# Performance work log

Hardware: AMD Instinct MI355X
Metric: run time of the kernel (lower is better)

The kernel has to match this reference:

```python
import jax, jax.numpy as jnp
import numpy as np

N, D, E, T = 30000, 256, 300000, 2
HID, OUT, HEADS = 64, 256, 8


def setup_inputs() -> dict:
    key = jax.random.key(0)
    ks = jax.random.split(key, 16)
    g = lambda k, shape, fan_in: jax.random.normal(k, shape, jnp.float32) / np.sqrt(fan_in)
    inp = {
        'x': jax.random.normal(ks[0], (N, D), jnp.float32),
        'edge_index': jax.random.randint(ks[1], (T, 2, E), 0, N, jnp.int32),
        'w1_l': g(ks[2], (T, D, HEADS * HID), D),
        'b1_l': jnp.zeros((T, HEADS * HID), jnp.float32),
        'w1_r': g(ks[3], (T, D, HEADS * HID), D),
        'b1_r': jnp.zeros((T, HEADS * HID), jnp.float32),
        'att1': g(ks[4], (T, HEADS, HID), HID),
        'bias1': jnp.zeros((T, HEADS * HID), jnp.float32),
        'w2_l': g(ks[5], (T, HEADS * HID, OUT), HEADS * HID),
        'b2_l': jnp.zeros((T, OUT), jnp.float32),
        'w2_r': g(ks[6], (T, HEADS * HID, OUT), HEADS * HID),
        'b2_r': jnp.zeros((T, OUT), jnp.float32),
        'att2': g(ks[7], (T, 1, OUT), OUT),
        'bias2': jnp.zeros((T, OUT), jnp.float32),
        'w_lin': g(ks[8], (OUT, OUT), OUT),
        'b_lin': jnp.zeros((OUT,), jnp.float32),
    }
    return inp


def _gatv2(x, src, dst, w_l, b_l, w_r, b_r, att, bias, num_nodes):
    # GATv2Conv: e = att . leaky_relu(W_l x_src + W_r x_dst); softmax over in-edges of dst;
    # out = scatter_add(alpha * W_l x_src) per destination; concat heads + bias.
    H, C = att.shape
    xl = (x @ w_l + b_l).reshape(num_nodes, H, C)
    xr = (x @ w_r + b_r).reshape(num_nodes, H, C)
    h = jax.nn.leaky_relu(xl[src] + xr[dst], 0.2)      # [E, H, C]
    e = jnp.einsum('ehc,hc->eh', h, att)               # [E, H]
    m = jax.ops.segment_max(e, dst, num_segments=num_nodes)
    p = jnp.exp(e - m[dst])
    s = jax.ops.segment_sum(p, dst, num_segments=num_nodes)
    alpha = p / s[dst]                                 # softmax over neighbors
    out = jax.ops.segment_sum(xl[src] * alpha[:, :, None], dst, num_segments=num_nodes)
    return out.reshape(num_nodes, H * C) + bias


def reference(x, edge_index, w1_l, b1_l, w1_r, b1_r, att1, bias1,
              w2_l, b2_l, w2_r, b2_r, att2, bias2, w_lin, b_lin):
    n = x.shape[0]
    loop = jnp.arange(n, dtype=edge_index.dtype)  # GATv2Conv default add_self_loops=True
    srcs, dsts = [], []
    for t in range(edge_index.shape[0]):
        srcs.append(jnp.concatenate([edge_index[t, 0], loop]))
        dsts.append(jnp.concatenate([edge_index[t, 1], loop]))

    # conv1 (heads=8, concat) with HeteroConv aggr='sum'
    h1 = jnp.zeros((n, w1_l.shape[2]), x.dtype)
    for t in range(len(srcs)):
        h1 = h1 + _gatv2(x, srcs[t], dsts[t], w1_l[t], b1_l[t], w1_r[t], b1_r[t], att1[t], bias1[t], n)
    h1 = jax.nn.elu(h1)

    # conv2 (heads=1, concat=False -> mean over 1 head == identity)
    h2 = jnp.zeros((n, w2_l.shape[2]), x.dtype)
    for t in range(len(srcs)):
        h2 = h2 + _gatv2(h1, srcs[t], dsts[t], w2_l[t], b2_l[t], w2_r[t], b2_r[t], att2[t], bias2[t], n)
    h2 = jax.nn.elu(h2)

    return h2 @ w_lin + b_lin
```

## Files before the change

### kernel.cpp

```cpp
#include <hip/hip_runtime.h>
#include <math.h>

#define N_NODES 30000
#define D_IN    256
#define E_EDGES 300000
#define T_TYPES 2
#define HEADS   8
#define HID     64
#define F1      512
#define OUT_F   256
#define EP      (E_EDGES + N_NODES)

typedef __attribute__((ext_vector_type(8))) short bf16x8;
typedef __attribute__((ext_vector_type(4))) float f32x4;

__device__ __forceinline__ unsigned short f2bf(float f) {
    unsigned u = __float_as_uint(f);
    unsigned r = 0x7fffu + ((u >> 16) & 1u);
    return (unsigned short)((u + r) >> 16);
}
__device__ __forceinline__ float bf2f(unsigned short h) {
    return __uint_as_float(((unsigned)h) << 16);
}

#define PREP_W1   (8 * 65536)
#define PREP_W2   (4 * 131072)
#define PREP_WL   65536
#define PREP_CNT  (T_TYPES * N_NODES)
#define PREP_TOT  (PREP_W1 + PREP_W2 + PREP_WL + PREP_CNT)

__global__ void prep_kernel(const float* __restrict__ w1_l, const float* __restrict__ w1_r,
                            const float* __restrict__ w2_l, const float* __restrict__ w2_r,
                            const float* __restrict__ w_lin,
                            unsigned short* __restrict__ wt1h, unsigned short* __restrict__ wt1l,
                            unsigned short* __restrict__ wt2h, unsigned short* __restrict__ wt2l,
                            unsigned short* __restrict__ wtLh, unsigned short* __restrict__ wtLl,
                            int* __restrict__ count) {
    int idx = blockIdx.x * blockDim.x + threadIdx.x;
    if (idx < PREP_W1) {
        int n = idx & 255, k = (idx >> 8) & 255, mat = idx >> 16;
        int h = mat & 1, lr = (mat >> 1) & 1, t = mat >> 2;
        const float* src = lr ? w1_r : w1_l;
        float v = src[(size_t)t * 256 * 512 + (size_t)k * 512 + h * 256 + n];
        unsigned short hi = f2bf(v);
        unsigned short lo = f2bf(v - bf2f(hi));
        size_t o = (size_t)mat * 65536 + (size_t)n * 256 + k;
        wt1h[o] = hi; wt1l[o] = lo;
        return;
    }
    idx -= PREP_W1;
    if (idx < PREP_W2) {
        int n = idx & 255, k = (idx >> 8) & 511, mat = idx >> 17;
        int lr = mat & 1, t = mat >> 1;
        const float* src = lr ? w2_r : w2_l;
        float v = src[(size_t)t * 512 * 256 + (size_t)k * 256 + n];
        unsigned short hi = f2bf(v);
        unsigned short lo = f2bf(v - bf2f(hi));
        size_t o = (size_t)mat * 131072 + (size_t)n * 512 + k;
        wt2h[o] = hi; wt2l[o] = lo;
        return;
    }
    idx -= PREP_W2;
    if (idx < PREP_WL) {
        int n = idx & 255, k = idx >> 8;
        float v = w_lin[k * 256 + n];
        unsigned short hi = f2bf(v);
        unsigned short lo = f2bf(v - bf2f(hi));
        size_t o = (size_t)n * 256 + k;
        wtLh[o] = hi; wtLl[o] = lo;
        return;
    }
    idx -= PREP_WL;
    if (idx < PREP_CNT) count[idx] = 0;
}

__global__ void hist_kernel(const int* __restrict__ ei, int* __restrict__ count) {
    int idx = blockIdx.x * blockDim.x + threadIdx.x;
    if (idx >= T_TYPES * EP) return;
    int t = idx / EP, i = idx - t * EP;
    int dst = (i < E_EDGES) ? ei[t * 2 * E_EDGES + E_EDGES + i] : (i - E_EDGES);
    atomicAdd(&count[t * N_NODES + dst], 1);
}

#define SCAN_NB 30

__global__ __launch_bounds__(256) void scan_bsum_kernel(const int* __restrict__ cnt,
                                                        int* __restrict__ bsum) {
    int t = blockIdx.y, b = blockIdx.x;
    const int* c = cnt + t * N_NODES;
    int i0 = b * 1024 + threadIdx.x * 4;
    int s = 0;
    #pragma unroll
    for (int j = 0; j < 4; ++j) { int i = i0 + j; if (i < N_NODES) s += c[i]; }
    #pragma unroll
    for (int m = 1; m < 64; m <<= 1) s += __shfl_xor(s, m);
    __shared__ int wsum[4];
    int l = threadIdx.x & 63, w = threadIdx.x >> 6;
    if (l == 0) wsum[w] = s;
    __syncthreads();
    if (threadIdx.x == 0) bsum[t * SCAN_NB + b] = wsum[0] + wsum[1] + wsum[2] + wsum[3];
}

__global__ void scan_base_kernel(int* __restrict__ bsum) {
    int t = threadIdx.x;
    if (t >= T_TYPES) return;
    int acc = 0;
    for (int b = 0; b < SCAN_NB; ++b) {
        int v = bsum[t * SCAN_NB + b];
        bsum[t * SCAN_NB + b] = acc;
        acc += v;
    }
}

__global__ __launch_bounds__(256) void scan_write_kernel(int* __restrict__ cnt,
                                                         const int* __restrict__ bsum,
                                                         int* __restrict__ off) {
    int t = blockIdx.y, b = blockIdx.x;
    int tid = threadIdx.x;
    int* c = cnt + t * N_NODES;
    int* o = off + t * (N_NODES + 1);
    int i0 = b * 1024 + tid * 4;
    int v[4]; int s = 0;
    #pragma unroll
    for (int j = 0; j < 4; ++j) { int i = i0 + j; v[j] = (i < N_NODES) ? c[i] : 0; s += v[j]; }
    __shared__ int ps[256];
    ps[tid] = s;
    __syncthreads();
    for (int ofs = 1; ofs < 256; ofs <<= 1) {
        int x = (tid >= ofs) ? ps[tid - ofs] : 0;
        __syncthreads();
        ps[tid] += x;
        __syncthreads();
    }
    int base = bsum[t * SCAN_NB + b] + ps[tid] - s;
    #pragma unroll
    for (int j = 0; j < 4; ++j) {
        int i = i0 + j;
        if (i < N_NODES) { o[i] = base; base += v[j]; c[i] = 0; }
    }
    if (b == 0 && tid == 0) o[N_NODES] = EP;
}

__global__ void scatter_kernel(const int* __restrict__ ei, const int* __restrict__ offsets,
                               int* __restrict__ cursor, int* __restrict__ csr_src) {
    int idx = blockIdx.x * blockDim.x + threadIdx.x;
    if (idx >= T_TYPES * EP) return;
    int t = idx / EP, i = idx - t * EP;
    int src, dst;
    if (i < E_EDGES) {
        src = ei[t * 2 * E_EDGES + i];
        dst = ei[t * 2 * E_EDGES + E_EDGES + i];
    } else {
        src = dst = i - E_EDGES;
    }
    int pos = offsets[t * (N_NODES + 1) + dst] + atomicAdd(&cursor[t * N_NODES + dst], 1);
    csr_src[t * EP + pos] = src;
}

__global__ __launch_bounds__(256) void gemm_mfma_kernel(
        const float* __restrict__ A, int lda,
        const unsigned short* __restrict__ Bh0, const unsigned short* __restrict__ Bl0,
        const float* __restrict__ bias0, float* __restrict__ C0,
        const unsigned short* __restrict__ Bh1, const unsigned short* __restrict__ Bl1,
        const float* __restrict__ bias1, float* __restrict__ C1,
        int M, int K) {
    const unsigned short* Bh = blockIdx.y ? Bh1 : Bh0;
    const unsigned short* Bl = blockIdx.y ? Bl1 : Bl0;
    const float* bias = blockIdx.y ? bias1 : bias0;
    float* C = blockIdx.y ? C1 : C0;

    __shared__ unsigned short Ah_s[64 * 32], Al_s[64 * 32];
    __shared__ unsigned short Bh_s[256 * 32], Bl_s[256 * 32];
    int t = threadIdx.x;
    int row0 = blockIdx.x * 64;
    int w = t >> 6;
    int l = t & 63;
    int fm = l & 15;
    int fg = l >> 4;

    f32x4 acc[4][4];
    const f32x4 zf = {0.f, 0.f, 0.f, 0.f};
    #pragma unroll
    for (int i = 0; i < 4; ++i)
        #pragma unroll
        for (int j = 0; j < 4; ++j) acc[i][j] = zf;

    int ar = t >> 3;
    int af = t & 7;
    int bn = t >> 2;
    int bb = t & 3;

    for (int k0 = 0; k0 < K; k0 += 32) {
        #pragma unroll
        for (int v = 0; v < 2; ++v) {
            int r = v * 32 + ar;
            int rg = row0 + r;
            float4 a4 = make_float4(0.f, 0.f, 0.f, 0.f);
            if (rg < M) a4 = *(const float4*)&A[(size_t)rg * lda + k0 + af * 4];
            ushort4 hi, lo;
            hi.x = f2bf(a4.x); lo.x = f2bf(a4.x - bf2f(hi.x));
            hi.y = f2bf(a4.y); lo.y = f2bf(a4.y - bf2f(hi.y));
            hi.z = f2bf(a4.z); lo.z = f2bf(a4.z - bf2f(hi.z));
            hi.w = f2bf(a4.w); lo.w = f2bf(a4.w - bf2f(hi.w));
            int ke = (af * 4) ^ (((r >> 1) & 3) << 3);
            *(ushort4*)&Ah_s[r * 32 + ke] = hi;
            *(ushort4*)&Al_s[r * 32 + ke] = lo;
        }
        #pragma unroll
        for (int g = 0; g < 4; ++g) {
            int n = g * 64 + bn;
            *(uint4*)&Bh_s[n * 32 + bb * 8] = *(const uint4*)&Bh[(size_t)n * K + k0 + bb * 8];
            *(uint4*)&Bl_s[n * 32 + bb * 8] = *(const uint4*)&Bl[(size_t)n * K + k0 + bb * 8];
        }
        __syncthreads();
        bf16x8 ah[4], al[4], bh[4], bl[4];
        #pragma unroll
        for (int i = 0; i < 4; ++i) {
            int r = i * 16 + fm;
            int ke = (fg * 8) ^ (((r >> 1) & 3) << 3);
            ah[i] = *(const bf16x8*)&Ah_s[r * 32 + ke];
            al[i] = *(const bf16x8*)&Al_s[r * 32 + ke];
        }
        #pragma unroll
        for (int j = 0; j < 4; ++j) {
            int n = w * 64 + j * 16 + fm;
            bh[j] = *(const bf16x8*)&Bh_s[n * 32 + fg * 8];
            bl[j] = *(const bf16x8*)&Bl_s[n * 32 + fg * 8];
        }
        #pragma unroll
        for (int i = 0; i < 4; ++i)
            #pragma unroll
            for (int j = 0; j < 4; ++j) {
                acc[i][j] = __builtin_amdgcn_mfma_f32_16x16x32_bf16(ah[i], bh[j], acc[i][j], 0, 0, 0);
                acc[i][j] = __builtin_amdgcn_mfma_f32_16x16x32_bf16(ah[i], bl[j], acc[i][j], 0, 0, 0);
                acc[i][j] = __builtin_amdgcn_mfma_f32_16x16x32_bf16(al[i], bh[j], acc[i][j], 0, 0, 0);
            }
        __syncthreads();
    }
    #pragma unroll
    for (int j = 0; j < 4; ++j) {
        int col = w * 64 + j * 16 + fm;
        float bv = bias[col];
        #pragma unroll
        for (int i = 0; i < 4; ++i) {
            #pragma unroll
            for (int q = 0; q < 4; ++q) {
                int rg = row0 + i * 16 + fg * 4 + q;
                if (rg < M) C[(size_t)rg * 256 + col] = acc[i][j][q] + bv;
            }
        }
    }
}

template <int RW, int MODE>
__global__ __launch_bounds__(256) void gat_edge_kernel(
        const float* __restrict__ xl, const float* __restrict__ xr,
        const float* __restrict__ att,
        const int* __restrict__ offs, const int* __restrict__ csr,
        float* __restrict__ out, int ldo,
        const float* __restrict__ eb0, const float* __restrict__ eb1) {
    int wave = (blockIdx.x * blockDim.x + threadIdx.x) >> 6;
    int lane = threadIdx.x & 63;
    if (wave >= N_NODES) return;
    int d = wave;
    int q4 = lane * 4;
    float attr[4], xrr[4];
    *(float4*)&attr[0] = *(const float4*)&att[q4];
    *(float4*)&xrr[0]  = *(const float4*)&xr[(size_t)d * 256 + q4];
    float m = -INFINITY, s = 0.f;
    float acc[4] = {0.f, 0.f, 0.f, 0.f};
    int p0 = offs[d], p1 = offs[d + 1];
    int p = p0;
    for (; p + 2 <= p1; p += 2) {
        int s0 = csr[p], s1 = csr[p + 1];
        float xv0[4], xv1[4];
        *(float4*)&xv0[0] = *(const float4*)&xl[(size_t)s0 * 256 + q4];
        *(float4*)&xv1[0] = *(const float4*)&xl[(size_t)s1 * 256 + q4];
        float e0 = 0.f, e1 = 0.f;
        #pragma unroll
        for (int q = 0; q < 4; ++q) {
            float h0 = xv0[q] + xrr[q];
            float h1 = xv1[q] + xrr[q];
            h0 = (h0 > 0.f) ? h0 : 0.2f * h0;
            h1 = (h1 > 0.f) ? h1 : 0.2f * h1;
            e0 += attr[q] * h0;
            e1 += attr[q] * h1;
        }
        #pragma unroll
        for (int msk = 1; msk < RW; msk <<= 1) {
            e0 += __shfl_xor(e0, msk);
            e1 += __shfl_xor(e1, msk);
        }
        float mn = fmaxf(m, e0);
        float sc = __expf(m - mn);
        float pe = __expf(e0 - mn);
        s = s * sc + pe;
        #pragma unroll
        for (int q = 0; q < 4; ++q) acc[q] = acc[q] * sc + pe * xv0[q];
        m = mn;
        mn = fmaxf(m, e1);
        sc = __expf(m - mn);
        pe = __expf(e1 - mn);
        s = s * sc + pe;
        #pragma unroll
        for (int q = 0; q < 4; ++q) acc[q] = acc[q] * sc + pe * xv1[q];
        m = mn;
    }
    if (p < p1) {
        int s0 = csr[p];
        float xv0[4];
        *(float4*)&xv0[0] = *(const float4*)&xl[(size_t)s0 * 256 + q4];
        float e0 = 0.f;
        #pragma unroll
        for (int q = 0; q < 4; ++q) {
            float h0 = xv0[q] + xrr[q];
            h0 = (h0 > 0.f) ? h0 : 0.2f * h0;
            e0 += attr[q] * h0;
        }
        #pragma unroll
        for (int msk = 1; msk < RW; msk <<= 1) e0 += __shfl_xor(e0, msk);
        float mn = fmaxf(m, e0);
        float sc = __expf(m - mn);
        float pe = __expf(e0 - mn);
        s = s * sc + pe;
        #pragma unroll
        for (int q = 0; q < 4; ++q) acc[q] = acc[q] * sc + pe * xv0[q];
        m = mn;
    }
    float inv = 1.f / s;
    float* dp = &out[(size_t)d * ldo + q4];
    if (MODE == 0) {
        *(float4*)dp = make_float4(acc[0] * inv, acc[1] * inv, acc[2] * inv, acc[3] * inv);
    } else {
        #pragma unroll
        for (int q = 0; q < 4; ++q) {
            float v = dp[q] + acc[q] * inv + eb0[q4 + q] + eb1[q4 + q];
            dp[q] = (v > 0.f) ? v : (__expf(v) - 1.f);
        }
    }
}

extern "C" void kernel_launch(void* const* d_in, const int* in_sizes, int n_in,
                              void* d_out, int out_size, void* d_ws, size_t ws_size,
                              hipStream_t stream) {
    const float* x      = (const float*)d_in[0];
    const int*   ei     = (const int*)d_in[1];
    const float* w1_l   = (const float*)d_in[2];
    const float* b1_l   = (const float*)d_in[3];
    const float* w1_r   = (const float*)d_in[4];
    const float* b1_r   = (const float*)d_in[5];
    const float* att1   = (const float*)d_in[6];
    const float* bias1  = (const float*)d_in[7];
    const float* w2_l   = (const float*)d_in[8];
    const float* b2_l   = (const float*)d_in[9];
    const float* w2_r   = (const float*)d_in[10];
    const float* b2_r   = (const float*)d_in[11];
    const float* att2   = (const float*)d_in[12];
    const float* bias2  = (const float*)d_in[13];
    const float* w_lin  = (const float*)d_in[14];
    const float* b_lin  = (const float*)d_in[15];
    float* out = (float*)d_out;

    float* h1   = (float*)d_ws;
    float* bufA = h1 + (size_t)N_NODES * F1;
    float* bufB = bufA + (size_t)N_NODES * OUT_F;
    unsigned short* wt1h = (unsigned short*)(bufB + (size_t)N_NODES * OUT_F);
    unsigned short* wt1l = wt1h + 8 * 65536;
    unsigned short* wt2h = wt1l + 8 * 65536;
    unsigned short* wt2l = wt2h + 4 * 131072;
    unsigned short* wtLh = wt2l + 4 * 131072;
    unsigned short* wtLl = wtLh + 65536;
    int* count   = (int*)(wtLl + 65536);
    int* offsets = count + T_TYPES * N_NODES;
    int* bsum    = offsets + T_TYPES * (N_NODES + 1);
    int* csr     = bsum + T_TYPES * SCAN_NB;
    float* h2 = out;

    prep_kernel<<<(PREP_TOT + 255) / 256, 256, 0, stream>>>(
        w1_l, w1_r, w2_l, w2_r, w_lin, wt1h, wt1l, wt2h, wt2l, wtLh, wtLl, count);

    int eblocks = (T_TYPES * EP + 255) / 256;
    hist_kernel<<<eblocks, 256, 0, stream>>>(ei, count);
    dim3 sgrid(SCAN_NB, T_TYPES);
    scan_bsum_kernel<<<sgrid, 256, 0, stream>>>(count, bsum);
    scan_base_kernel<<<1, 64, 0, stream>>>(bsum);
    scan_write_kernel<<<sgrid, 256, 0, stream>>>(count, bsum, offsets);
    scatter_kernel<<<eblocks, 256, 0, stream>>>(ei, offsets, count, csr);

    int gat_blocks = N_NODES / 4;
    dim3 ggrid((N_NODES + 63) / 64, 2);
    dim3 ggrid1((N_NODES + 63) / 64, 1);

    for (int t = 0; t < T_TYPES; ++t) {
        for (int hh = 0; hh < 2; ++hh) {
            int co = hh * 256;
            int ml = (t * 2 + 0) * 2 + hh, mr = (t * 2 + 1) * 2 + hh;
            gemm_mfma_kernel<<<ggrid, 256, 0, stream>>>(
                x, D_IN,
                wt1h + (size_t)ml * 65536, wt1l + (size_t)ml * 65536, b1_l + t * F1 + co, bufA,
                wt1h + (size_t)mr * 65536, wt1l + (size_t)mr * 65536, b1_r + t * F1 + co, bufB,
                N_NODES, D_IN);
            if (t == 0)
                gat_edge_kernel<16, 0><<<gat_blocks, 256, 0, stream>>>(
                    bufA, bufB, att1 + t * F1 + co, offsets + t * (N_NODES + 1),
                    csr + (size_t)t * EP, h1 + co, F1, nullptr, nullptr);
            else
                gat_edge_kernel<16, 2><<<gat_blocks, 256, 0, stream>>>(
                    bufA, bufB, att1 + t * F1 + co, offsets + t * (N_NODES + 1),
                    csr + (size_t)t * EP, h1 + co, F1, bias1 + co, bias1 + F1 + co);
        }
    }

    for (int t = 0; t < T_TYPES; ++t) {
        int ml = t * 2 + 0, mr = t * 2 + 1;
        gemm_mfma_kernel<<<ggrid, 256, 0, stream>>>(
            h1, F1,
            wt2h + (size_t)ml * 131072, wt2l + (size_t)ml * 131072, b2_l + t * OUT_F, bufA,
            wt2h + (size_t)mr * 131072, wt2l + (size_t)mr * 131072, b2_r + t * OUT_F, bufB,
            N_NODES, F1);
        if (t == 0)
            gat_edge_kernel<64, 0><<<gat_blocks, 256, 0, stream>>>(
                bufA, bufB, att2 + t * OUT_F, offsets + t * (N_NODES + 1),
                csr + (size_t)t * EP, h2, OUT_F, nullptr, nullptr);
        else
            gat_edge_kernel<64, 2><<<gat_blocks, 256, 0, stream>>>(
                bufA, bufB, att2 + t * OUT_F, offsets + t * (N_NODES + 1),
                csr + (size_t)t * EP, h2, OUT_F, bias2, bias2 + OUT_F);
    }

    hipMemcpyAsync(bufA, h2, (size_t)N_NODES * OUT_F * sizeof(float),
                   hipMemcpyDeviceToDevice, stream);
    gemm_mfma_kernel<<<ggrid1, 256, 0, stream>>>(
        bufA, OUT_F, wtLh, wtLl, b_lin, out, wtLh, wtLl, b_lin, out, N_NODES, OUT_F);
}
```

Measured before the change: 905.5 us.

## Register-prefetch GEMM tiles, swizzle B in LDS, and emit split-bf16 h2 from the edge kernel

The GEMM kernel now loads the next K-tile of A and B into registers while computing the current one, overlapping global loads with MFMA work. It also XOR-swizzles the B tile in shared memory to avoid bank conflicts and adds a launch-bounds occupancy hint. The last GAT edge kernel writes h2 directly as pre-split bf16 hi/lo arrays, so the final linear GEMM reads them without conversion and the device-to-device copy is removed. In exchange, register pressure rises from the prefetch buffers, and h1 storage is reused to hold the split h2.

Result: slower. 1.480 ms (+63.4%).

```diff
diff --git a/kernel.cpp b/kernel.cpp
--- a/kernel.cpp
+++ b/kernel.cpp
@@ -157,8 +157,9 @@
     csr_src[t * EP + pos] = src;
 }
 
-__global__ __launch_bounds__(256) void gemm_mfma_kernel(
-        const float* __restrict__ A, int lda,
+template <int ASPLIT>
+__global__ __launch_bounds__(256, 3) void gemm_mfma_kernel(
+        const void* __restrict__ A0v, const void* __restrict__ A1v, int lda,
         const unsigned short* __restrict__ Bh0, const unsigned short* __restrict__ Bl0,
         const float* __restrict__ bias0, float* __restrict__ C0,
         const unsigned short* __restrict__ Bh1, const unsigned short* __restrict__ Bl1,
@@ -168,6 +169,9 @@
     const unsigned short* Bl = blockIdx.y ? Bl1 : Bl0;
     const float* bias = blockIdx.y ? bias1 : bias0;
     float* C = blockIdx.y ? C1 : C0;
+    const float* Af          = (const float*)A0v;
+    const unsigned short* Ah = (const unsigned short*)A0v;
+    const unsigned short* Al = (const unsigned short*)A1v;
 
     __shared__ unsigned short Ah_s[64 * 32], Al_s[64 * 32];
     __shared__ unsigned short Bh_s[256 * 32], Bl_s[256 * 32];
@@ -185,55 +189,90 @@
         #pragma unroll
         for (int j = 0; j < 4; ++j) acc[i][j] = zf;
 
-    int ar = t >> 3;
-    int af = t & 7;
-    int bn = t >> 2;
-    int bb = t & 3;
-
-    for (int k0 = 0; k0 < K; k0 += 32) {
-        #pragma unroll
-        for (int v = 0; v < 2; ++v) {
-            int r = v * 32 + ar;
-            int rg = row0 + r;
-            float4 a4 = make_float4(0.f, 0.f, 0.f, 0.f);
-            if (rg < M) a4 = *(const float4*)&A[(size_t)rg * lda + k0 + af * 4];
-            ushort4 hi, lo;
-            hi.x = f2bf(a4.x); lo.x = f2bf(a4.x - bf2f(hi.x));
-            hi.y = f2bf(a4.y); lo.y = f2bf(a4.y - bf2f(hi.y));
-            hi.z = f2bf(a4.z); lo.z = f2bf(a4.z - bf2f(hi.z));
-            hi.w = f2bf(a4.w); lo.w = f2bf(a4.w - bf2f(hi.w));
-            int ke = (af * 4) ^ (((r >> 1) & 3) << 3);
-            *(ushort4*)&Ah_s[r * 32 + ke] = hi;
-            *(ushort4*)&Al_s[r * 32 + ke] = lo;
+    int ar = t >> 3, af = t & 7;
+    int ar1 = t >> 2, ac1 = t & 3;
+    int bn = t >> 2, bb = t & 3;
+
+    float4 aP[2];
+    uint4 ahP, alP;
+    uint4 bhP[4], blP[4];
+
+    auto load_tile = [&](int k0) {
+        if constexpr (ASPLIT == 0) {
+            #pragma unroll
+            for (int v = 0; v < 2; ++v) {
+                int rg = row0 + v * 32 + ar;
+                aP[v] = make_float4(0.f, 0.f, 0.f, 0.f);
+                if (rg < M) aP[v] = *(const float4*)&Af[(size_t)rg * lda + k0 + af * 4];
+            }
+        } else {
+            int rg = row0 + ar1;
+            ahP = make_uint4(0, 0, 0, 0);
+            alP = make_uint4(0, 0, 0, 0);
+            if (rg < M) {
+                ahP = *(const uint4*)&Ah[(size_t)rg * lda + k0 + ac1 * 8];
+                alP = *(const uint4*)&Al[(size_t)rg * lda + k0 + ac1 * 8];
+            }
         }
         #pragma unroll
         for (int g = 0; g < 4; ++g) {
             int n = g * 64 + bn;
-            *(uint4*)&Bh_s[n * 32 + bb * 8] = *(const uint4*)&Bh[(size_t)n * K + k0 + bb * 8];
-            *(uint4*)&Bl_s[n * 32 + bb * 8] = *(const uint4*)&Bl[(size_t)n * K + k0 + bb * 8];
-        }
+            bhP[g] = *(const uint4*)&Bh[(size_t)n * K + k0 + bb * 8];
+            blP[g] = *(const uint4*)&Bl[(size_t)n * K + k0 + bb * 8];
+        }
+    };
+
+    load_tile(0);
+    for (int k0 = 0; k0 < K; k0 += 32) {
+        if constexpr (ASPLIT == 0) {
+            #pragma unroll
+            for (int v = 0; v < 2; ++v) {
+                int r = v * 32 + ar;
+                ushort4 hi, lo;
+                hi.x = f2bf(aP[v].x); lo.x = f2bf(aP[v].x - bf2f(hi.x));
+                hi.y = f2bf(aP[v].y); lo.y = f2bf(aP[v].y - bf2f(hi.y));
+                hi.z = f2bf(aP[v].z); lo.z = f2bf(aP[v].z - bf2f(hi.z));
+                hi.w = f2bf(aP[v].w); lo.w = f2bf(aP[v].w - bf2f(hi.w));
+                int ke = (af * 4) ^ (((r >> 1) & 3) << 3);
+                *(ushort4*)&Ah_s[r * 32 + ke] = hi;
+                *(ushort4*)&Al_s[r * 32 + ke] = lo;
+            }
+        } else {
+            int ke = (ac1 * 8) ^ (((ar1 >> 1) & 3) << 3);
+            *(uint4*)&Ah_s[ar1 * 32 + ke] = ahP;
+            *(uint4*)&Al_s[ar1 * 32 + ke] = alP;
+        }
+        #pragma unroll
+        for (int g = 0; g < 4; ++g) {
+            int n = g * 64 + bn;
+            int ke = (bb * 8) ^ (((n >> 1) & 3) << 3);
+            *(uint4*)&Bh_s[n * 32 + ke] = bhP[g];
+            *(uint4*)&Bl_s[n * 32 + ke] = blP[g];
+        }
+        if (k0 + 32 < K) load_tile(k0 + 32);
         __syncthreads();
-        bf16x8 ah[4], al[4], bh[4], bl[4];
+        bf16x8 ahf[4], alf[4], bhf[4], blf[4];
         #pragma unroll
         for (int i = 0; i < 4; ++i) {
             int r = i * 16 + fm;
             int ke = (fg * 8) ^ (((r >> 1) & 3) << 3);
-            ah[i] = *(const bf16x8*)&Ah_s[r * 32 + ke];
-            al[i] = *(const bf16x8*)&Al_s[r * 32 + ke];
+            ahf[i] = *(const bf16x8*)&Ah_s[r * 32 + ke];
+            alf[i] = *(const bf16x8*)&Al_s[r * 32 + ke];
         }
         #pragma unroll
         for (int j = 0; j < 4; ++j) {
             int n = w * 64 + j * 16 + fm;
-            bh[j] = *(const bf16x8*)&Bh_s[n * 32 + fg * 8];
-            bl[j] = *(const bf16x8*)&Bl_s[n * 32 + fg * 8];
+            int ke = (fg * 8) ^ (((n >> 1) & 3) << 3);
+            bhf[j] = *(const bf16x8*)&Bh_s[n * 32 + ke];
+            blf[j] = *(const bf16x8*)&Bl_s[n * 32 + ke];
         }
         #pragma unroll
         for (int i = 0; i < 4; ++i)
             #pragma unroll
             for (int j = 0; j < 4; ++j) {
-                acc[i][j] = __builtin_amdgcn_mfma_f32_16x16x32_bf16(ah[i], bh[j], acc[i][j], 0, 0, 0);
-                acc[i][j] = __builtin_amdgcn_mfma_f32_16x16x32_bf16(ah[i], bl[j], acc[i][j], 0, 0, 0);
-                acc[i][j] = __builtin_amdgcn_mfma_f32_16x16x32_bf16(al[i], bh[j], acc[i][j], 0, 0, 0);
+                acc[i][j] = __builtin_amdgcn_mfma_f32_16x16x32_bf16(ahf[i], bhf[j], acc[i][j], 0, 0, 0);
+                acc[i][j] = __builtin_amdgcn_mfma_f32_16x16x32_bf16(ahf[i], blf[j], acc[i][j], 0, 0, 0);
+                acc[i][j] = __builtin_amdgcn_mfma_f32_16x16x32_bf16(alf[i], bhf[j], acc[i][j], 0, 0, 0);
             }
         __syncthreads();
     }
@@ -258,7 +297,8 @@
         const float* __restrict__ att,
         const int* __restrict__ offs, const int* __restrict__ csr,
         float* __restrict__ out, int ldo,
-        const float* __restrict__ eb0, const float* __restrict__ eb1) {
+        const float* __restrict__ eb0, const float* __restrict__ eb1,
+        unsigned short* __restrict__ sh, unsigned short* __restrict__ sl) {
     int wave = (blockIdx.x * blockDim.x + threadIdx.x) >> 6;
     int lane = threadIdx.x & 63;
     if (wave >= N_NODES) return;
@@ -331,12 +371,28 @@
     float* dp = &out[(size_t)d * ldo + q4];
     if (MODE == 0) {
         *(float4*)dp = make_float4(acc[0] * inv, acc[1] * inv, acc[2] * inv, acc[3] * inv);
-    } else {
+    } else if (MODE == 2) {
         #pragma unroll
         for (int q = 0; q < 4; ++q) {
             float v = dp[q] + acc[q] * inv + eb0[q4 + q] + eb1[q4 + q];
             dp[q] = (v > 0.f) ? v : (__expf(v) - 1.f);
         }
+    } else {
+        ushort4 hv, lv;
+        float v0 = dp[0] + acc[0] * inv + eb0[q4 + 0] + eb1[q4 + 0];
+        float v1 = dp[1] + acc[1] * inv + eb0[q4 + 1] + eb1[q4 + 1];
+        float v2 = dp[2] + acc[2] * inv + eb0[q4 + 2] + eb1[q4 + 2];
+        float v3 = dp[3] + acc[3] * inv + eb0[q4 + 3] + eb1[q4 + 3];
+        v0 = (v0 > 0.f) ? v0 : (__expf(v0) - 1.f);
+        v1 = (v1 > 0.f) ? v1 : (__expf(v1) - 1.f);
+        v2 = (v2 > 0.f) ? v2 : (__expf(v2) - 1.f);
+        v3 = (v3 > 0.f) ? v3 : (__expf(v3) - 1.f);
+        hv.x = f2bf(v0); lv.x = f2bf(v0 - bf2f(hv.x));
+        hv.y = f2bf(v1); lv.y = f2bf(v1 - bf2f(hv.y));
+        hv.z = f2bf(v2); lv.z = f2bf(v2 - bf2f(hv.z));
+        hv.w = f2bf(v3); lv.w = f2bf(v3 - bf2f(hv.w));
+        *(ushort4*)&sh[(size_t)d * ldo + q4] = hv;
+        *(ushort4*)&sl[(size_t)d * ldo + q4] = lv;
     }
 }
 
@@ -374,7 +430,8 @@
     int* offsets = count + T_TYPES * N_NODES;
     int* bsum    = offsets + T_TYPES * (N_NODES + 1);
     int* csr     = bsum + T_TYPES * SCAN_NB;
-    float* h2 = out;
+    unsigned short* h2s_hi = (unsigned short*)h1;
+    unsigned short* h2s_lo = h2s_hi + (size_t)N_NODES * OUT_F;
 
     prep_kernel<<<(PREP_TOT + 255) / 256, 256, 0, stream>>>(
         w1_l, w1_r, w2_l, w2_r, w_lin, wt1h, wt1l, wt2h, wt2l, wtLh, wtLl, count);
@@ -395,41 +452,44 @@
         for (int hh = 0; hh < 2; ++hh) {
             int co = hh * 256;
             int ml = (t * 2 + 0) * 2 + hh, mr = (t * 2 + 1) * 2 + hh;
-            gemm_mfma_kernel<<<ggrid, 256, 0, stream>>>(
-                x, D_IN,
+            gemm_mfma_kernel<0><<<ggrid, 256, 0, stream>>>(
+                x, nullptr, D_IN,
                 wt1h + (size_t)ml * 65536, wt1l + (size_t)ml * 65536, b1_l + t * F1 + co, bufA,
                 wt1h + (size_t)mr * 65536, wt1l + (size_t)mr * 65536, b1_r + t * F1 + co, bufB,
                 N_NODES, D_IN);
             if (t == 0)
                 gat_edge_kernel<16, 0><<<gat_blocks, 256, 0, stream>>>(
                     bufA, bufB, att1 + t * F1 + co, offsets + t * (N_NODES + 1),
-                    csr + (size_t)t * EP, h1 + co, F1, nullptr, nullptr);
+                    csr + (size_t)t * EP, h1 + co, F1, nullptr, nullptr, nullptr, nullptr);
             else
                 gat_edge_kernel<16, 2><<<gat_blocks, 256, 0, stream>>>(
                     bufA, bufB, att1 + t * F1 + co, offsets + t * (N_NODES + 1),
-                    csr + (size_t)t * EP, h1 + co, F1, bias1 + co, bias1 + F1 + co);
+                    csr + (size_t)t * EP, h1 + co, F1, bias1 + co, bias1 + F1 + co,
+                    nullptr, nullptr);
         }
     }
 
     for (int t = 0; t < T_TYPES; ++t) {
         int ml = t * 2 + 0, mr = t * 2 + 1;
-        gemm_mfma_kernel<<<ggrid, 256, 0, stream>>>(
-            h1, F1,
+        gemm_mfma_kernel<0><<<ggrid, 256, 0, stream>>>(
+            h1, nullptr, F1,
             wt2h + (size_t)ml * 131072, wt2l + (size_t)ml * 131072, b2_l + t * OUT_F, bufA,
             wt2h + (size_t)mr * 131072, wt2l + (size_t)mr * 131072, b2_r + t * OUT_F, bufB,
             N_NODES, F1);
         if (t == 0)
             gat_edge_kernel<64, 0><<<gat_blocks, 256, 0, stream>>>(
                 bufA, bufB, att2 + t * OUT_F, offsets + t * (N_NODES + 1),
-                csr + (size_t)t * EP, h2, OUT_F, nullptr, nullptr);
+                csr + (size_t)t * EP, out, OUT_F, nullptr, nullptr, nullptr, nullptr);
         else
-            gat_edge_kernel<64, 2><<<gat_blocks, 256, 0, stream>>>(
+            gat_edge_kernel<64, 3><<<gat_blocks, 256, 0, stream>>>(
                 bufA, bufB, att2 + t * OUT_F, offsets + t * (N_NODES + 1),
-                csr + (size_t)t * EP, h2, OUT_F, bias2, bias2 + OUT_F);
-    }
-
-    hipMemcpyAsync(bufA, h2, (size_t)N_NODES * OUT_F * sizeof(float),
-                   hipMemcpyDeviceToDevice, stream);
-    gemm_mfma_kernel<<<ggrid1, 256, 0, stream>>>(
-        bufA, OUT_F, wtLh, wtLl, b_lin, out, wtLh, wtLl, b_lin, out, N_NODES, OUT_F);
-}
+                csr + (size_t)t * EP, out, OUT_F, bias2, bias2 + OUT_F,
+                h2s_hi, h2s_lo);
+    }
+
+    gemm_mfma_kernel<1><<<ggrid1, 256, 0, stream>>>(
+        h2s_hi, h2s_lo, OUT_F,
+        wtLh, wtLl, b_lin, out,
+        wtLh, wtLl, b_lin, out,
+        N_NODES, OUT_F);
+}
```
